# Kernel optimization log

Measured on AMD Instinct MI355X. Metric: run time of the kernel, lower is better.

The kernel has to match this reference:

```python
import jax, jax.numpy as jnp
import numpy as np

MASK_VALUE = float(-2**32 + 1)  # additive fill used by the torch module
B, QT, KT, D = 16, 2048, 2048, 1024


def setup_inputs() -> dict:
    key = jax.random.key(0)
    kq, kk, kv, kql, kkl = jax.random.split(key, 5)
    return {
        "Q": jax.random.normal(kq, (B, QT, D), dtype=jnp.float32),
        "K": jax.random.normal(kk, (B, KT, D), dtype=jnp.float32),
        "V": jax.random.normal(kv, (B, KT, D), dtype=jnp.float32),
        "Q_lengths": jax.random.randint(kql, (B,), 1, QT + 1, dtype=jnp.int32),
        "K_lengths": jax.random.randint(kkl, (B,), 1, KT + 1, dtype=jnp.int32),
    }


def reference(Q, K, V, Q_lengths, K_lengths):
    # dot-product scores: [b, qt, kt]
    logits = jnp.einsum("bqd,bkd->bqk", Q, K)
    # length mask: outer product of row-valid and col-valid masks
    q_valid = (jnp.arange(Q.shape[1]) < Q_lengths[:, None]).astype(logits.dtype)  # [b, qt]
    k_valid = (jnp.arange(K.shape[1]) < K_lengths[:, None]).astype(logits.dtype)  # [b, kt]
    mask = q_valid[:, :, None] * k_valid[:, None, :]                               # [b, qt, kt]
    logits = mask * logits + (1.0 - mask) * MASK_VALUE
    attention = jax.nn.softmax(logits, axis=-1)
    return jnp.einsum("bqk,bkd->bqd", attention, V)
```

## Files before the change

### kernel.cpp

```cpp
#include <hip/hip_runtime.h>

#define BATCH 16
#define QT    2048
#define KTOT  2048
#define DIM   1024
#define NITEMS (BATCH * (QT / 32))

typedef __attribute__((ext_vector_type(8))) _Float16 f16x8;
typedef __attribute__((ext_vector_type(4))) _Float16 f16x4;
typedef __attribute__((ext_vector_type(2))) _Float16 f16x2;
typedef __attribute__((ext_vector_type(4))) float    f32x4;
typedef __attribute__((ext_vector_type(2))) float    f32x2;

__global__ __launch_bounds__(256) void conv_k(const float* __restrict__ K,
                                              _Float16* __restrict__ Kf) {
    const size_t idx = ((size_t)blockIdx.x * 256 + threadIdx.x) * 8;
    f32x4 a0 = *(const f32x4*)(K + idx);
    f32x4 a1 = *(const f32x4*)(K + idx + 4);
    f16x8 h;
#pragma unroll
    for (int j = 0; j < 4; ++j) { h[j] = (_Float16)a0[j]; h[4 + j] = (_Float16)a1[j]; }
    *(f16x8*)(Kf + idx) = h;
}

__global__ __launch_bounds__(256) void trans_v(const float* __restrict__ V,
                                               _Float16* __restrict__ Vt) {
    const int blk = blockIdx.x;
    const int b   = blk >> 9;
    const int kt0 = ((blk >> 4) & 31) << 6;
    const int d0  = (blk & 15) << 6;
    __shared__ _Float16 tbuf[64][65];
    const int tid = threadIdx.x;
    const int cr  = tid >> 4;
    const int c4  = (tid & 15) << 2;
#pragma unroll
    for (int p = 0; p < 4; ++p) {
        const int r = cr + p * 16;
        f32x4 v = *(const f32x4*)(V + ((size_t)(b * KTOT + kt0 + r)) * DIM + d0 + c4);
#pragma unroll
        for (int j = 0; j < 4; ++j) tbuf[r][c4 + j] = (_Float16)v[j];
    }
    __syncthreads();
#pragma unroll
    for (int p = 0; p < 4; ++p) {
        const int dr = cr + p * 16;
        f16x4 o;
#pragma unroll
        for (int j = 0; j < 4; ++j) o[j] = tbuf[c4 + j][dr];
        *(f16x4*)(Vt + ((size_t)(b * DIM + d0 + dr)) * KTOT + kt0 + c4) = o;
    }
}

__global__ __launch_bounds__(256) void fill_mean_vt(const _Float16* __restrict__ Vt,
                                                    const int* __restrict__ Qlen,
                                                    float* __restrict__ out) {
    const int gid  = blockIdx.x * 256 + threadIdx.x;
    const int row  = gid >> 2;
    const int part = gid & 3;
    const int b = row >> 10, d = row & 1023;
    const f16x8* src = (const f16x8*)(Vt + (size_t)row * KTOT) + part * (KTOT / 32);
    float s = 0.0f;
    for (int i = 0; i < KTOT / 32; ++i) {
        f16x8 v = src[i];
#pragma unroll
        for (int j = 0; j < 8; ++j) s += (float)v[j];
    }
    s += __shfl_xor(s, 1, 64);
    s += __shfl_xor(s, 2, 64);
    const float mv = s * (1.0f / (float)KTOT);
    const int qlen = Qlen[b];
    for (int q = qlen + part; q < QT; q += 4)
        out[((size_t)(b * QT + q)) * DIM + d] = mv;
}

__global__ __launch_bounds__(512, 2) void attn_main(
    const float* __restrict__ Q, const int* __restrict__ Qlen, const int* __restrict__ Klen,
    const _Float16* __restrict__ Kf, const _Float16* __restrict__ Vt,
    float* __restrict__ out, unsigned* __restrict__ counter) {

    __shared__ float    sred[2][8][32][34];
    __shared__ _Float16 pbuf[2][32][40];
    __shared__ float    arow[2][32];
    __shared__ float    lrow[32];
    __shared__ unsigned item_s;

    const int tid  = threadIdx.x;
    const int w    = tid >> 6;
    const int ln   = tid & 63;
    const int l16  = ln & 15;
    const int quad = ln >> 4;
    const int d0   = w << 7;
    const int sr  = tid >> 4;
    const int scg = tid & 15;

    const unsigned bxcd = (unsigned)(blockIdx.x & 7);
    unsigned gx = bxcd;
    int goff = 0;

    for (;;) {
        __syncthreads();
        if (tid == 0) {
            unsigned pick = 0xFFFFFFFFu;
            while (goff < 8) {
                unsigned it = atomicAdd(&counter[gx], 1u);
                if (it < 128u) { pick = gx * 128u + it; break; }
                ++goff;
                gx = (bxcd + (unsigned)goff) & 7u;
            }
            item_s = pick;
        }
        __syncthreads();
        const unsigned item = item_s;
        if (item == 0xFFFFFFFFu) break;
        const int grp  = (int)(item >> 7);
        const int ii   = (int)(item & 127u);
        const int b    = (grp << 1) + (ii >> 6);
        const int qt   = (ii & 63) << 5;
        const int qlen = Qlen[b];
        if (qt >= qlen) continue;
        const int klen = Klen[b];
        const int nkt  = (klen + 31) >> 5;

        f16x8 qh[2][4], ql[2][4];
#pragma unroll
        for (int mi = 0; mi < 2; ++mi)
#pragma unroll
            for (int kc = 0; kc < 4; ++kc) {
                const float* src = Q + ((size_t)(b * QT + qt + mi * 16 + l16)) * DIM
                                     + d0 + kc * 32 + quad * 8;
                f32x4 a0 = *(const f32x4*)src;
                f32x4 a1 = *(const f32x4*)(src + 4);
                f16x8 h, l;
#pragma unroll
                for (int j = 0; j < 4; ++j) {
                    _Float16 h0 = (_Float16)a0[j];
                    h[j] = h0; l[j] = (_Float16)(a0[j] - (float)h0);
                    _Float16 h1 = (_Float16)a1[j];
                    h[4 + j] = h1; l[4 + j] = (_Float16)(a1[j] - (float)h1);
                }
                qh[mi][kc] = h; ql[mi][kc] = l;
            }

        f32x4 o[2][8];
        const f32x4 fzero = {0.0f, 0.0f, 0.0f, 0.0f};
#pragma unroll
        for (int mi = 0; mi < 2; ++mi)
#pragma unroll
            for (int nd = 0; nd < 8; ++nd) o[mi][nd] = fzero;

        float msx = -3.0e38f, lsx = 0.0f;

        f16x8 kf[2][4];
        {
            const _Float16* kb = Kf + ((size_t)(b * KTOT + l16)) * DIM + d0 + quad * 8;
#pragma unroll
            for (int ni = 0; ni < 2; ++ni)
#pragma unroll
                for (int kc = 0; kc < 4; ++kc)
                    kf[ni][kc] = *(const f16x8*)(kb + (size_t)(ni * 16) * DIM + kc * 32);
        }

        f16x8 vf[8];

        for (int t = 0; t <= nkt; ++t) {
            const int cur = t & 1, prv = cur ^ 1;

            if (t < nkt) {
                f32x4 s00 = fzero, s01 = fzero, s10 = fzero, s11 = fzero;
#pragma unroll
                for (int kc = 0; kc < 4; ++kc) {
                    s00 = __builtin_amdgcn_mfma_f32_16x16x32_f16(qh[0][kc], kf[0][kc], s00, 0, 0, 0);
                    s10 = __builtin_amdgcn_mfma_f32_16x16x32_f16(qh[1][kc], kf[0][kc], s10, 0, 0, 0);
                    s00 = __builtin_amdgcn_mfma_f32_16x16x32_f16(ql[0][kc], kf[0][kc], s00, 0, 0, 0);
                    s10 = __builtin_amdgcn_mfma_f32_16x16x32_f16(ql[1][kc], kf[0][kc], s10, 0, 0, 0);
                    s01 = __builtin_amdgcn_mfma_f32_16x16x32_f16(qh[0][kc], kf[1][kc], s01, 0, 0, 0);
                    s11 = __builtin_amdgcn_mfma_f32_16x16x32_f16(qh[1][kc], kf[1][kc], s11, 0, 0, 0);
                    s01 = __builtin_amdgcn_mfma_f32_16x16x32_f16(ql[0][kc], kf[1][kc], s01, 0, 0, 0);
                    s11 = __builtin_amdgcn_mfma_f32_16x16x32_f16(ql[1][kc], kf[1][kc], s11, 0, 0, 0);
                }
#pragma unroll
                for (int r2 = 0; r2 < 4; ++r2) {
                    sred[cur][w][quad * 4 + r2][l16]           = s00[r2];
                    sred[cur][w][quad * 4 + r2][16 + l16]      = s01[r2];
                    sred[cur][w][16 + quad * 4 + r2][l16]      = s10[r2];
                    sred[cur][w][16 + quad * 4 + r2][16 + l16] = s11[r2];
                }
            }

            if (t > 0) {
                const int kt0p = (t - 1) << 5;
                const int c0 = scg * 2, c1 = c0 + 1;
                float x0 = 0.0f, x1 = 0.0f;
#pragma unroll
                for (int ww = 0; ww < 8; ++ww) {
                    f32x2 xp = *(const f32x2*)&sred[prv][ww][sr][c0];
                    x0 += xp[0]; x1 += xp[1];
                }
                if (kt0p + c0 >= klen) x0 = -3.0e38f;
                if (kt0p + c1 >= klen) x1 = -3.0e38f;
                float pm = fmaxf(x0, x1);
#pragma unroll
                for (int off = 1; off < 16; off <<= 1) pm = fmaxf(pm, __shfl_xor(pm, off, 64));
                const float mn    = fmaxf(msx, pm);
                const float alpha = __expf(msx - mn);
                const float p0 = __expf(x0 - mn), p1 = __expf(x1 - mn);
                float ps = p0 + p1;
#pragma unroll
                for (int off = 1; off < 16; off <<= 1) ps += __shfl_xor(ps, off, 64);
                lsx = lsx * alpha + ps;
                msx = mn;
                f16x2 pw; pw[0] = (_Float16)p0; pw[1] = (_Float16)p1;
                *(f16x2*)&pbuf[prv][sr][c0] = pw;
                if (scg == 0) arow[prv][sr] = alpha;
            }

            if (t + 1 < nkt) {
                const int ktn = (t + 1) << 5;
                const _Float16* kb = Kf + ((size_t)(b * KTOT + ktn + l16)) * DIM
                                        + d0 + quad * 8;
#pragma unroll
                for (int ni = 0; ni < 2; ++ni)
#pragma unroll
                    for (int kc = 0; kc < 4; ++kc)
                        kf[ni][kc] = *(const f16x8*)(kb + (size_t)(ni * 16) * DIM + kc * 32);
            }

            __syncthreads();

            if (t > 0) {
                f32x4 av0 = *(const f32x4*)&arow[prv][quad * 4];
                f32x4 av1 = *(const f32x4*)&arow[prv][16 + quad * 4];
#pragma unroll
                for (int nd = 0; nd < 8; ++nd) { o[0][nd] *= av0; o[1][nd] *= av1; }

                f16x8 pa0 = *(const f16x8*)&pbuf[prv][l16][quad * 8];
                f16x8 pa1 = *(const f16x8*)&pbuf[prv][16 + l16][quad * 8];
#pragma unroll
                for (int nd = 0; nd < 8; ++nd) {
                    o[0][nd] = __builtin_amdgcn_mfma_f32_16x16x32_f16(pa0, vf[nd], o[0][nd], 0, 0, 0);
                    o[1][nd] = __builtin_amdgcn_mfma_f32_16x16x32_f16(pa1, vf[nd], o[1][nd], 0, 0, 0);
                }
            }

            if (t < nkt) {
                const int kt0v = t << 5;
#pragma unroll
                for (int nd = 0; nd < 8; ++nd)
                    vf[nd] = *(const f16x8*)(Vt + ((size_t)(b * DIM + d0 + nd * 16 + l16)) * KTOT
                                             + kt0v + quad * 8);
            }
        }

        if (scg == 0) lrow[sr] = lsx;
        __syncthreads();
        f32x4 li0, li1;
#pragma unroll
        for (int r2 = 0; r2 < 4; ++r2) {
            li0[r2] = 1.0f / lrow[quad * 4 + r2];
            li1[r2] = 1.0f / lrow[16 + quad * 4 + r2];
        }
#pragma unroll
        for (int mi = 0; mi < 2; ++mi)
#pragma unroll
            for (int r2 = 0; r2 < 4; ++r2) {
                const int row = qt + mi * 16 + quad * 4 + r2;
                if (row < qlen) {
                    const float inv = mi ? li1[r2] : li0[r2];
#pragma unroll
                    for (int nd = 0; nd < 8; ++nd)
                        out[((size_t)(b * QT + row)) * DIM + d0 + nd * 16 + l16] =
                            o[mi][nd][r2] * inv;
                }
            }
    }
}

__global__ __launch_bounds__(256) void fill_mean_f32(const float* __restrict__ V,
                                                     const int* __restrict__ Qlen,
                                                     float* __restrict__ out) {
    const int b  = blockIdx.x >> 4;
    const int d0 = (blockIdx.x & 15) << 6;
    const int qlen = Qlen[b];
    const int tid = threadIdx.x;
    const int dc = d0 + (tid & 63);
    const int part = tid >> 6;
    __shared__ float red[4][64];
    __shared__ float mcol[64];
    float sm = 0.0f;
    for (int kt = part; kt < KTOT; kt += 4)
        sm += V[((size_t)(b * KTOT + kt)) * DIM + dc];
    red[part][tid & 63] = sm;
    __syncthreads();
    if (tid < 64)
        mcol[tid] = (red[0][tid] + red[1][tid] + red[2][tid] + red[3][tid]) * (1.0f / (float)KTOT);
    __syncthreads();
    const float mv = mcol[tid & 63];
    for (int q = qlen + part; q < QT; q += 4)
        out[((size_t)(b * QT + q)) * DIM + dc] = mv;
}

__global__ __launch_bounds__(512) void attn_naive(
    const float* __restrict__ Q, const float* __restrict__ K, const float* __restrict__ V,
    const int* __restrict__ Qlen, const int* __restrict__ Klen, float* __restrict__ out) {
    const int blk  = blockIdx.x;
    const int b    = blk >> 8;
    const int qb   = (blk & 255) << 3;
    const int qlen = Qlen[b];
    if (qb >= qlen) return;
    const int klen = Klen[b];
    const int tid  = threadIdx.x;
    const int wid  = tid >> 6, ln = tid & 63;
    const int q    = qb + wid;
    __shared__ float kbuf[1024], vbuf[1024];
    f32x4 qr[4];
#pragma unroll
    for (int i = 0; i < 4; ++i)
        qr[i] = *(const f32x4*)(Q + ((size_t)(b * QT + q)) * DIM + i * 256 + ln * 4);
    const f32x4 fzero = {0.0f, 0.0f, 0.0f, 0.0f};
    f32x4 acc[4] = {fzero, fzero, fzero, fzero};
    float m = -3.0e38f, l = 0.0f;
    for (int kt = 0; kt < klen; ++kt) {
        __syncthreads();
        if (tid < 256)
            *(f32x4*)&kbuf[tid * 4] = *(const f32x4*)(K + ((size_t)(b * KTOT + kt)) * DIM + tid * 4);
        else
            *(f32x4*)&vbuf[(tid - 256) * 4] =
                *(const f32x4*)(V + ((size_t)(b * KTOT + kt)) * DIM + (tid - 256) * 4);
        __syncthreads();
        float sp = 0.0f;
#pragma unroll
        for (int i = 0; i < 4; ++i) {
            f32x4 kv = *(const f32x4*)&kbuf[i * 256 + ln * 4];
            sp += qr[i][0] * kv[0] + qr[i][1] * kv[1] + qr[i][2] * kv[2] + qr[i][3] * kv[3];
        }
#pragma unroll
        for (int off = 1; off < 64; off <<= 1) sp += __shfl_xor(sp, off, 64);
        const float mn = fmaxf(m, sp);
        const float a  = __expf(m - mn);
        const float p  = __expf(sp - mn);
        l = l * a + p; m = mn;
#pragma unroll
        for (int i = 0; i < 4; ++i) {
            f32x4 vv = *(const f32x4*)&vbuf[i * 256 + ln * 4];
            acc[i] = acc[i] * a + vv * p;
        }
    }
    if (q < qlen) {
        const float inv = 1.0f / l;
#pragma unroll
        for (int i = 0; i < 4; ++i)
            *(f32x4*)(out + ((size_t)(b * QT + q)) * DIM + i * 256 + ln * 4) = acc[i] * inv;
    }
}

extern "C" void kernel_launch(void* const* d_in, const int* in_sizes, int n_in,
                              void* d_out, int out_size, void* d_ws, size_t ws_size,
                              hipStream_t stream) {
    (void)in_sizes; (void)n_in; (void)out_size;
    const float* Q    = (const float*)d_in[0];
    const float* K    = (const float*)d_in[1];
    const float* V    = (const float*)d_in[2];
    const int*   Qlen = (const int*)d_in[3];
    const int*   Klen = (const int*)d_in[4];
    float*       out  = (float*)d_out;

    const size_t HALF = (size_t)BATCH * KTOT * DIM;
    const size_t NEED = HALF * 2  * sizeof(_Float16) + 64;
    if (ws_size >= NEED) {
        _Float16* kf = (_Float16*)d_ws;
        _Float16* vt = kf + HALF;
        unsigned* ctr = (unsigned*)((char*)d_ws + HALF * 2 * sizeof(_Float16));
        hipMemsetAsync(ctr, 0, 8 * sizeof(unsigned), stream);
        conv_k<<<dim3(16384), dim3(256), 0, stream>>>(K, kf);
        trans_v<<<dim3(8192), dim3(256), 0, stream>>>(V, vt);
        fill_mean_vt<<<dim3(256), dim3(256), 0, stream>>>(vt, Qlen, out);
        attn_main<<<dim3(256), dim3(512), 0, stream>>>(Q, Qlen, Klen, kf, vt, out, ctr);
    } else {
        fill_mean_f32<<<dim3(BATCH * 16), dim3(256), 0, stream>>>(V, Qlen, out);
        attn_naive<<<dim3(4096), dim3(512), 0, stream>>>(Q, K, V, Qlen, Klen, out);
    }
}
```

Baseline: 740.6 us.

## Use DPP row reductions, defer sum reduction, hoist K prefetch, skip unit rescale

Replaces the shuffle-based 16-lane max and sum reductions in the online softmax with DPP row permutes. The per-tile sum reduction is removed: each lane keeps a partial running sum, and a single reduction runs at the end. The next K tile prefetch now issues right after the QK MFMAs so its latency overlaps the softmax stage. The O accumulator rescale is skipped when every alpha in the wave equals one. This trims cross-lane communication and VALU work per tile, at the cost of a wave-wide vote and branch plus earlier register pressure from the hoisted loads.

```diff
diff --git a/kernel.cpp b/kernel.cpp
--- a/kernel.cpp
+++ b/kernel.cpp
@@ -11,6 +11,27 @@
 typedef __attribute__((ext_vector_type(2))) _Float16 f16x2;
 typedef __attribute__((ext_vector_type(4))) float    f32x4;
 typedef __attribute__((ext_vector_type(2))) float    f32x2;
+
+template <int CTRL>
+__device__ __forceinline__ float dpp_perm(float x) {
+    int i = __builtin_bit_cast(int, x);
+    int r = __builtin_amdgcn_update_dpp(i, i, CTRL, 0xF, 0xF, true);
+    return __builtin_bit_cast(float, r);
+}
+__device__ __forceinline__ float row16_allmax(float x) {
+    x = fmaxf(x, dpp_perm<0xB1>(x));
+    x = fmaxf(x, dpp_perm<0x4E>(x));
+    x = fmaxf(x, dpp_perm<0x141>(x));
+    x = fmaxf(x, dpp_perm<0x128>(x));
+    return x;
+}
+__device__ __forceinline__ float row16_allsum(float x) {
+    x = x + dpp_perm<0xB1>(x);
+    x = x + dpp_perm<0x4E>(x);
+    x = x + dpp_perm<0x141>(x);
+    x = x + dpp_perm<0x128>(x);
+    return x;
+}
 
 __global__ __launch_bounds__(256) void conv_k(const float* __restrict__ K,
                                               _Float16* __restrict__ Kf) {
@@ -178,6 +199,18 @@
                     s01 = __builtin_amdgcn_mfma_f32_16x16x32_f16(ql[0][kc], kf[1][kc], s01, 0, 0, 0);
                     s11 = __builtin_amdgcn_mfma_f32_16x16x32_f16(ql[1][kc], kf[1][kc], s11, 0, 0, 0);
                 }
+
+                if (t + 1 < nkt) {
+                    const int ktn = (t + 1) << 5;
+                    const _Float16* kb = Kf + ((size_t)(b * KTOT + ktn + l16)) * DIM
+                                            + d0 + quad * 8;
+#pragma unroll
+                    for (int ni = 0; ni < 2; ++ni)
+#pragma unroll
+                        for (int kc = 0; kc < 4; ++kc)
+                            kf[ni][kc] = *(const f16x8*)(kb + (size_t)(ni * 16) * DIM + kc * 32);
+                }
+
 #pragma unroll
                 for (int r2 = 0; r2 < 4; ++r2) {
                     sred[cur][w][quad * 4 + r2][l16]           = s00[r2];
@@ -198,40 +231,30 @@
                 }
                 if (kt0p + c0 >= klen) x0 = -3.0e38f;
                 if (kt0p + c1 >= klen) x1 = -3.0e38f;
-                float pm = fmaxf(x0, x1);
-#pragma unroll
-                for (int off = 1; off < 16; off <<= 1) pm = fmaxf(pm, __shfl_xor(pm, off, 64));
+                const float pm = row16_allmax(fmaxf(x0, x1));
                 const float mn    = fmaxf(msx, pm);
                 const float alpha = __expf(msx - mn);
                 const float p0 = __expf(x0 - mn), p1 = __expf(x1 - mn);
-                float ps = p0 + p1;
-#pragma unroll
-                for (int off = 1; off < 16; off <<= 1) ps += __shfl_xor(ps, off, 64);
-                lsx = lsx * alpha + ps;
+                lsx = lsx * alpha + (p0 + p1);
                 msx = mn;
                 f16x2 pw; pw[0] = (_Float16)p0; pw[1] = (_Float16)p1;
                 *(f16x2*)&pbuf[prv][sr][c0] = pw;
                 if (scg == 0) arow[prv][sr] = alpha;
             }
 
-            if (t + 1 < nkt) {
-                const int ktn = (t + 1) << 5;
-                const _Float16* kb = Kf + ((size_t)(b * KTOT + ktn + l16)) * DIM
-                                        + d0 + quad * 8;
-#pragma unroll
-                for (int ni = 0; ni < 2; ++ni)
-#pragma unroll
-                    for (int kc = 0; kc < 4; ++kc)
-                        kf[ni][kc] = *(const f16x8*)(kb + (size_t)(ni * 16) * DIM + kc * 32);
-            }
-
             __syncthreads();
 
             if (t > 0) {
                 f32x4 av0 = *(const f32x4*)&arow[prv][quad * 4];
                 f32x4 av1 = *(const f32x4*)&arow[prv][16 + quad * 4];
-#pragma unroll
-                for (int nd = 0; nd < 8; ++nd) { o[0][nd] *= av0; o[1][nd] *= av1; }
+                bool needr = false;
+#pragma unroll
+                for (int j = 0; j < 4; ++j)
+                    needr = needr || (av0[j] != 1.0f) || (av1[j] != 1.0f);
+                if (__any(needr)) {
+#pragma unroll
+                    for (int nd = 0; nd < 8; ++nd) { o[0][nd] *= av0; o[1][nd] *= av1; }
+                }
 
                 f16x8 pa0 = *(const f16x8*)&pbuf[prv][l16][quad * 8];
                 f16x8 pa1 = *(const f16x8*)&pbuf[prv][16 + l16][quad * 8];
@@ -251,7 +274,10 @@
             }
         }
 
-        if (scg == 0) lrow[sr] = lsx;
+        {
+            const float lt = row16_allsum(lsx);
+            if (scg == 0) lrow[sr] = lt;
+        }
         __syncthreads();
         f32x4 li0, li1;
 #pragma unroll
```

Result: no change. 747.3 us (+0.9%).
